# Performance work log

Measured on AMD Instinct MI355X. Metric: run time of the kernel, lower is better.

Reference implementation:

```python
import jax, jax.numpy as jnp
import numpy as np

EMBED_DIM = 256
NUM_HEADS = 8
HEAD_DIM = EMBED_DIM // NUM_HEADS


def setup_inputs() -> dict:
    key0 = jax.random.key(0)
    ks = jax.random.split(key0, 12)
    B, T, S, E = 4, 256, 16384, EMBED_DIM
    inv = 1.0 / np.sqrt(E)
    inputs = {
        "query": jax.random.normal(ks[0], (B, T, E), dtype=jnp.float32),
        "key": jax.random.normal(ks[1], (B, S, E), dtype=jnp.float32),
        "value": jax.random.normal(ks[2], (B, S, E), dtype=jnp.float32),
        "mask": jax.random.uniform(ks[3], (B, T, S), dtype=jnp.float32),
        # nn.MultiheadAttention in-projection (split into q/k/v parts) and out-projection
        "Wq": jax.random.uniform(ks[4], (E, E), jnp.float32, -inv, inv),
        "bq": jnp.zeros((E,), jnp.float32),
        "Wk": jax.random.uniform(ks[5], (E, E), jnp.float32, -inv, inv),
        "bk": jnp.zeros((E,), jnp.float32),
        "Wv": jax.random.uniform(ks[6], (E, E), jnp.float32, -inv, inv),
        "bv": jnp.zeros((E,), jnp.float32),
        "Wo": jax.random.uniform(ks[7], (E, E), jnp.float32, -inv, inv),
        "bo": jnp.zeros((E,), jnp.float32),
        # fixed default scaling factors (num_heads must be 8)
        "scaling_factors": jnp.asarray([32.0, 32.0, 16.0, 16.0, 8.0, 8.0, 4.0, 4.0], jnp.float32),
    }
    return inputs


def reference(query, key, value, mask, Wq, bq, Wk, bk, Wv, bv, Wo, bo, scaling_factors):
    B, T, E = query.shape
    S = key.shape[1]
    H, D = NUM_HEADS, HEAD_DIM
    # input projections (torch Linear convention: x @ W.T + b)
    q = (query @ Wq.T + bq).reshape(B, T, H, D).transpose(0, 2, 1, 3)  # [B,H,T,D]
    k = (key @ Wk.T + bk).reshape(B, S, H, D).transpose(0, 2, 1, 3)    # [B,H,S,D]
    v = (value @ Wv.T + bv).reshape(B, S, H, D).transpose(0, 2, 1, 3)  # [B,H,S,D]
    scale = 1.0 / jnp.sqrt(jnp.asarray(D, query.dtype))
    scores = jnp.einsum("bhtd,bhsd->bhts", q * scale, k)               # [B,H,T,S]
    # per-head scaled soft mask added as attention bias
    bias = mask[:, None, :, :] * scaling_factors[None, :, None, None]  # [B,H,T,S]
    attn = jax.nn.softmax(scores + bias, axis=-1)
    out = jnp.einsum("bhts,bhsd->bhtd", attn, v)                       # [B,H,T,D]
    out = out.transpose(0, 2, 1, 3).reshape(B, T, E)
    return out @ Wo.T + bo
```

## Files before the change

### kernel.cpp

```cpp
#include <hip/hip_runtime.h>

#define B_ 4
#define T_ 256
#define S_ 16384
#define E_ 256
#define H_ 8
#define D_ 32

typedef _Float16 f16;
typedef _Float16 f16x2 __attribute__((ext_vector_type(2)));
typedef _Float16 f16x4 __attribute__((ext_vector_type(4)));
typedef _Float16 f16x8 __attribute__((ext_vector_type(8)));
typedef float f32x4 __attribute__((ext_vector_type(4)));

typedef const __attribute__((address_space(1))) void* gas_t;
typedef __attribute__((address_space(3))) void* las_t;

__device__ __forceinline__ void gload_lds16(const void* g, void* l) {
    __builtin_amdgcn_global_load_lds((gas_t)g, (las_t)l, 16, 0, 0);
}

__device__ __forceinline__ f16x2 cvt_pk_f16(float a, float b) {
    return __builtin_bit_cast(f16x2, __builtin_amdgcn_cvt_pkrtz(a, b));
}

#define LOG2E 1.4426950408889634f

__global__ void cvt_w4_kernel(const float* __restrict__ wa, const float* __restrict__ wb,
                              const float* __restrict__ wc, const float* __restrict__ wd,
                              f16* __restrict__ oa, f16* __restrict__ ob,
                              f16* __restrict__ oc, f16* __restrict__ od) {
    int m = blockIdx.y;
    const float* src = m == 0 ? wa : m == 1 ? wb : m == 2 ? wc : wd;
    f16* dst = m == 0 ? oa : m == 1 ? ob : m == 2 ? oc : od;
    int i = (blockIdx.x * 256 + threadIdx.x) * 4;
    float4 v = *(const float4*)(src + i);
    f16x4 h = {(f16)v.x, (f16)v.y, (f16)v.z, (f16)v.w};
    *(f16x4*)(dst + i) = h;
}

template <bool OUT16>
__device__ __forceinline__ void qproj_body(
    f16* SMEM, const float* __restrict__ in, const f16* __restrict__ w16,
    const float* __restrict__ bias, void* __restrict__ outp, int bid, float oscale)
{
    f16 (*As)[264] = (f16(*)[264])SMEM;
    f16 (*Bs)[264] = (f16(*)[264])(SMEM + 32 * 264);
    int tid = threadIdx.x;
    int wq = tid >> 6, ln = tid & 63, g = ln >> 4, lc = ln & 15;
    int row0 = (bid & 31) * 32;
    int n0 = (bid >> 5) * 32;
    {
        int r = tid >> 3, q0 = (tid & 7) * 32;
        const float* ip = in + (size_t)(row0 + r) * 256 + q0;
        #pragma unroll
        for (int i = 0; i < 8; i++) {
            float4 v = *(const float4*)(ip + i * 4);
            f16x4 hv = {(f16)v.x, (f16)v.y, (f16)v.z, (f16)v.w};
            *(f16x4*)&As[r][q0 + i * 4] = hv;
        }
        const f16* wp = w16 + (size_t)(n0 + r) * 256 + q0;
        #pragma unroll
        for (int i = 0; i < 4; i++)
            *(f16x8*)&Bs[r][q0 + i * 8] = *(const f16x8*)(wp + i * 8);
    }
    __syncthreads();
    int mi = wq >> 1, ni = wq & 1;
    f32x4 acc = {0.f, 0.f, 0.f, 0.f};
    #pragma unroll
    for (int ks = 0; ks < 8; ks++) {
        f16x8 a = *(const f16x8*)&As[mi * 16 + lc][ks * 32 + g * 8];
        f16x8 bf = *(const f16x8*)&Bs[ni * 16 + lc][ks * 32 + g * 8];
        acc = __builtin_amdgcn_mfma_f32_16x16x32_f16(a, bf, acc, 0, 0, 0);
    }
    int n = n0 + ni * 16 + lc;
    float bv = bias[n];
    #pragma unroll
    for (int r = 0; r < 4; r++) {
        int row = row0 + mi * 16 + g * 4 + r;
        float val = (acc[r] + bv) * oscale;
        if (OUT16) ((f16*)outp)[(size_t)row * 256 + n] = (f16)val;
        else       ((float*)outp)[(size_t)row * 256 + n] = val;
    }
}

template <int MODE>
__device__ __forceinline__ void proj_body(
    f16* SMEM, const float* __restrict__ in, const f16* __restrict__ w16,
    const float* __restrict__ bias, void* __restrict__ outp, int bx, float oscale)
{
    f16 (*As)[64][40] = (f16(*)[64][40])&SMEM[0];
    f16* BsF = &SMEM[5120];
    int tid = threadIdx.x;
    int wv = tid >> 6, ln = tid & 63, g = ln >> 4, lc = ln & 15;
    int row0 = bx * 64;

    f32x4 acc[4][4];
    #pragma unroll
    for (int i = 0; i < 4; i++)
        #pragma unroll
        for (int j = 0; j < 4; j++) acc[i][j] = (f32x4){0.f, 0.f, 0.f, 0.f};

    auto stage = [&](int kb, int bufi) {
        int m = tid >> 3, kq = (tid & 7) << 2;
        #pragma unroll
        for (int h2 = 0; h2 < 2; h2++) {
            int mm = m + h2 * 32;
            float4 v = *(const float4*)(in + (size_t)(row0 + mm) * 256 + kb + kq);
            f16x4 hv = {(f16)v.x, (f16)v.y, (f16)v.z, (f16)v.w};
            *(f16x4*)&As[bufi][mm][kq] = hv;
        }
        #pragma unroll
        for (int c4 = 0; c4 < 4; c4++) {
            int cc = wv * 4 + c4;
            int row = cc * 16 + (ln >> 2);
            int sj = (ln & 3) ^ ((row >> 1) & 3);
            gload_lds16(w16 + (size_t)row * 256 + kb + sj * 8,
                        (char*)BsF + bufi * 16384 + cc * 1024);
        }
    };

    stage(0, 0);
    __syncthreads();
    #pragma unroll 1
    for (int ks = 0; ks < 8; ks++) {
        if (ks < 7) stage((ks + 1) * 32, (ks + 1) & 1);
        int bufi = ks & 1;
        f16x8 af[4], bf[4];
        #pragma unroll
        for (int mi = 0; mi < 4; mi++) af[mi] = *(const f16x8*)&As[bufi][mi * 16 + lc][g * 8];
        #pragma unroll
        for (int ni = 0; ni < 4; ni++) {
            int n = wv * 64 + ni * 16 + lc;
            bf[ni] = *(const f16x8*)&BsF[bufi * 8192 + n * 32 + ((g ^ ((n >> 1) & 3)) << 3)];
        }
        #pragma unroll
        for (int mi = 0; mi < 4; mi++)
            #pragma unroll
            for (int ni = 0; ni < 4; ni++)
                acc[mi][ni] = __builtin_amdgcn_mfma_f32_16x16x32_f16(af[mi], bf[ni], acc[mi][ni], 0, 0, 0);
        __syncthreads();
    }

    if (MODE == 1) {
        #pragma unroll
        for (int ni = 0; ni < 4; ni++) {
            int n = wv * 64 + ni * 16 + lc;
            float bv = bias[n];
            #pragma unroll
            for (int mi = 0; mi < 4; mi++) {
                #pragma unroll
                for (int r = 0; r < 4; r++) {
                    int row = row0 + mi * 16 + g * 4 + r;
                    ((f16*)outp)[(size_t)row * 256 + n] = (f16)((acc[mi][ni][r] + bv) * oscale);
                }
            }
        }
    } else {
        f16* TR = &SMEM[0];
        __syncthreads();
        #pragma unroll
        for (int ni = 0; ni < 4; ni++) {
            int n = wv * 64 + ni * 16 + lc;
            float bv = bias[n];
            #pragma unroll
            for (int mi = 0; mi < 4; mi++) {
                f16x4 hv;
                #pragma unroll
                for (int r = 0; r < 4; r++) hv[r] = (f16)((acc[mi][ni][r] + bv) * oscale);
                *(f16x4*)&TR[n * 68 + mi * 16 + g * 4] = hv;
            }
        }
        __syncthreads();
        int bb = row0 >> 14, sbase = row0 & 16383;
        f16* vout = (f16*)outp;
        #pragma unroll
        for (int p = 0; p < 4; p++) {
            int n = p * 64 + wv * 16 + (ln >> 2);
            int sc = (ln & 3) * 16;
            f16x8 v0 = *(const f16x8*)&TR[n * 68 + sc];
            f16x8 v1 = *(const f16x8*)&TR[n * 68 + sc + 8];
            f16* op = vout + ((size_t)(bb * 256 + n)) * 16384 + sbase + sc;
            *(f16x8*)op = v0;
            *(f16x8*)(op + 8) = v1;
        }
    }
}

__global__ __launch_bounds__(256, 3) void proj_fused(
    const float* __restrict__ query, const float* __restrict__ key, const float* __restrict__ value,
    const f16* __restrict__ Wq16, const f16* __restrict__ Wk16, const f16* __restrict__ Wv16,
    const float* __restrict__ bq, const float* __restrict__ bk, const float* __restrict__ bv,
    f16* __restrict__ q16, f16* __restrict__ k16, f16* __restrict__ v16T, float qscale)
{
    __shared__ __align__(16) f16 SMEM[21504];
    int bx = blockIdx.x;
    if (bx < 1024) {
        proj_body<1>(SMEM, key, Wk16, bk, k16, bx, 1.0f);
    } else if (bx < 2048) {
        proj_body<2>(SMEM, value, Wv16, bv, v16T, bx - 1024, 1.0f);
    } else {
        qproj_body<true>(SMEM, query, Wq16, bq, q16, bx - 2048, qscale);
    }
}

__global__ __launch_bounds__(256, 4) void out_proj(
    const float* __restrict__ in, const f16* __restrict__ w16,
    const float* __restrict__ bias, void* __restrict__ outp)
{
    __shared__ __align__(16) f16 SMEM[16896];
    qproj_body<false>(SMEM, in, w16, bias, outp, blockIdx.x + blockIdx.y * 32, 1.0f);
}

__global__ __launch_bounds__(1024, 4) void attn_kernel(
    const f16* __restrict__ q16,
    const f16* __restrict__ k16,
    const f16* __restrict__ v16T,
    const float* __restrict__ mask,
    const float* __restrict__ scal,
    float* __restrict__ partO, float* __restrict__ partL)
{
    constexpr int ITERS = 16;
    __shared__ __align__(16) f16 KT[3][32 * 256];
    __shared__ __align__(16) f16 VT[3][256 * 32];
    __shared__ __align__(16) float MT[3][128 * 32];

    int raw = blockIdx.x;
    int th = raw >> 7, b = (raw >> 5) & 3, ck = raw & 31;
    int tid = threadIdx.x;
    int wv = tid >> 6;
    int h = wv & 7, tsub = wv >> 3;
    int ln = tid & 63, g = ln >> 4, lc = ln & 15;
    int t0 = th * 128, s0 = ck * 512;

    float sc_h = scal[h] * LOG2E;
    float negfix = -(sc_h + 4.0f);

    f16x8 qf[4];
    #pragma unroll
    for (int tl = 0; tl < 4; tl++) {
        const f16* qp = q16 + (size_t)(b * T_ + t0 + tsub * 64 + tl * 16 + lc) * E_ + h * 32 + g * 8;
        qf[tl] = *(const f16x8*)qp;
    }

    f32x4 oac[4][2];
    float l_part[4];
    #pragma unroll
    for (int tl = 0; tl < 4; tl++) {
        oac[tl][0] = (f32x4){0.f, 0.f, 0.f, 0.f};
        oac[tl][1] = (f32x4){0.f, 0.f, 0.f, 0.f};
        l_part[tl] = 0.f;
    }

    auto stage = [&](int it, int bufi) {
        int sg0 = s0 + it * 32;
        {
            int sl = wv * 2 + (ln >> 5);
            int slot = (sl ^ (sl >> 3)) & 7;
            int jc = (ln & 31) ^ slot;
            gload_lds16(k16 + (size_t)(b * S_ + sg0 + sl) * E_ + jc * 8,
                        (char*)&KT[bufi][0] + wv * 1024);
        }
        {
            int dl = wv * 16 + (ln >> 2);
            int srcj = (ln & 3) ^ ((dl >> 1) & 3);
            gload_lds16(v16T + (size_t)(b * E_ + dl) * S_ + sg0 + srcj * 8,
                        (char*)&VT[bufi][0] + wv * 1024);
        }
        {
            int r = ln >> 3;
            int sj = (ln & 7) ^ r;
            gload_lds16(mask + (size_t)(b * T_ + t0 + wv * 8 + r) * S_ + sg0 + sj * 4,
                        (char*)&MT[bufi][0] + wv * 1024);
        }
    };

    stage(0, 0);
    stage(1, 1);

    f32x4 zero4 = {0.f, 0.f, 0.f, 0.f};
    int ib = 0;

    #pragma unroll 1
    for (int it = 0; it < ITERS; it++) {
        if (it + 1 < ITERS) { asm volatile("s_waitcnt vmcnt(3)" ::: "memory"); }
        else                { asm volatile("s_waitcnt vmcnt(0)" ::: "memory"); }
        __builtin_amdgcn_s_barrier();
        asm volatile("" ::: "memory");
        if (it + 2 < ITERS) {
            int wb = ib + 2; if (wb >= 3) wb -= 3;
            stage(it + 2, wb);
        }

        f16x8 kb[2];
        #pragma unroll
        for (int si = 0; si < 2; si++) {
            int sl = si * 16 + lc;
            int slot = (sl ^ (sl >> 3)) & 7;
            int j = (h * 4 + g) ^ slot;
            kb[si] = *(const f16x8*)((char*)&KT[ib][0] + sl * 512 + j * 16);
        }
        f16x4 va[2][2];
        #pragma unroll
        for (int si = 0; si < 2; si++) {
            #pragma unroll
            for (int ni = 0; ni < 2; ni++) {
                int d = h * 32 + ni * 16 + lc;
                int u = (si * 2 + (g >> 1)) ^ ((d >> 1) & 3);
                va[si][ni] = *(const f16x4*)((char*)&VT[ib][0] + d * 64 + u * 16 + (g & 1) * 8);
            }
        }

        #pragma unroll
        for (int tl = 0; tl < 4; tl++) {
            int t = tsub * 64 + tl * 16 + lc;
            const float4 mf0 = *(const float4*)((char*)&MT[ib][0] + t * 128 + (((g    ) ^ (t & 7)) << 4));
            const float4 mf1 = *(const float4*)((char*)&MT[ib][0] + t * 128 + (((4 + g) ^ (t & 7)) << 4));
            f32x4 st0 = __builtin_amdgcn_mfma_f32_16x16x32_f16(kb[0], qf[tl], zero4, 0, 0, 0);
            f32x4 st1 = __builtin_amdgcn_mfma_f32_16x16x32_f16(kb[1], qf[tl], zero4, 0, 0, 0);
            float p0 = __builtin_amdgcn_exp2f(st0[0] + __builtin_fmaf(mf0.x, sc_h, negfix));
            float p1 = __builtin_amdgcn_exp2f(st0[1] + __builtin_fmaf(mf0.y, sc_h, negfix));
            float p2 = __builtin_amdgcn_exp2f(st0[2] + __builtin_fmaf(mf0.z, sc_h, negfix));
            float p3 = __builtin_amdgcn_exp2f(st0[3] + __builtin_fmaf(mf0.w, sc_h, negfix));
            float p4 = __builtin_amdgcn_exp2f(st1[0] + __builtin_fmaf(mf1.x, sc_h, negfix));
            float p5 = __builtin_amdgcn_exp2f(st1[1] + __builtin_fmaf(mf1.y, sc_h, negfix));
            float p6 = __builtin_amdgcn_exp2f(st1[2] + __builtin_fmaf(mf1.z, sc_h, negfix));
            float p7 = __builtin_amdgcn_exp2f(st1[3] + __builtin_fmaf(mf1.w, sc_h, negfix));
            l_part[tl] += ((p0 + p1) + (p2 + p3)) + ((p4 + p5) + (p6 + p7));
            f16x2 c01 = cvt_pk_f16(p0, p1);
            f16x2 c23 = cvt_pk_f16(p2, p3);
            f16x2 c45 = cvt_pk_f16(p4, p5);
            f16x2 c67 = cvt_pk_f16(p6, p7);
            f16x4 pb0 = {c01[0], c01[1], c23[0], c23[1]};
            f16x4 pb1 = {c45[0], c45[1], c67[0], c67[1]};
            oac[tl][0] = __builtin_amdgcn_mfma_f32_16x16x16f16(va[0][0], pb0, oac[tl][0], 0, 0, 0);
            oac[tl][0] = __builtin_amdgcn_mfma_f32_16x16x16f16(va[1][0], pb1, oac[tl][0], 0, 0, 0);
            oac[tl][1] = __builtin_amdgcn_mfma_f32_16x16x16f16(va[0][1], pb0, oac[tl][1], 0, 0, 0);
            oac[tl][1] = __builtin_amdgcn_mfma_f32_16x16x16f16(va[1][1], pb1, oac[tl][1], 0, 0, 0);
        }
        ib++; if (ib >= 3) ib -= 3;
    }

    #pragma unroll
    for (int tl = 0; tl < 4; tl++) {
        float lv = l_part[tl];
        lv += __shfl_xor(lv, 16, 64);
        lv += __shfl_xor(lv, 32, 64);
        l_part[tl] = lv;
    }
    float* po = partO + (size_t)raw * 128 * 256;
    #pragma unroll
    for (int tl = 0; tl < 4; tl++) {
        #pragma unroll
        for (int ni = 0; ni < 2; ni++) {
            float4 o4 = {oac[tl][ni][0], oac[tl][ni][1], oac[tl][ni][2], oac[tl][ni][3]};
            *(float4*)(po + (size_t)(tsub * 64 + tl * 16 + lc) * 256 + h * 32 + ni * 16 + g * 4) = o4;
        }
    }
    if (g == 0) {
        float* pl = partL + (size_t)raw * 128 * 8;
        #pragma unroll
        for (int tl = 0; tl < 4; tl++) {
            int trow = tsub * 64 + tl * 16 + lc;
            pl[trow * 8 + h] = l_part[tl];
        }
    }
}

__global__ __launch_bounds__(256) void combine_kernel(
    const float* __restrict__ partO, const float* __restrict__ partL,
    float* __restrict__ attnO)
{
    int bid = blockIdx.x;
    int b = bid >> 8, t = bid & 255;
    int th = t >> 7, tl = t & 127;
    int tid = threadIdx.x;
    __shared__ float sl[32][8];
    {
        int ck = tid >> 3, hh = tid & 7;
        size_t blk = (size_t)(th * 128 + b * 32 + ck);
        sl[ck][hh] = partL[blk * 1024 + tl * 8 + hh];
    }
    __syncthreads();
    int h = tid >> 5;
    float L = 0.f;
    #pragma unroll 8
    for (int ck = 0; ck < 32; ck++) L += sl[ck][h];
    float acc = 0.f;
    #pragma unroll 4
    for (int ck = 0; ck < 32; ck++) {
        size_t blk = (size_t)(th * 128 + b * 32 + ck);
        acc += partO[blk * 32768 + (size_t)tl * 256 + tid];
    }
    attnO[(size_t)bid * 256 + tid] = acc / L;
}

extern "C" void kernel_launch(void* const* d_in, const int* in_sizes, int n_in,
                              void* d_out, int out_size, void* d_ws, size_t ws_size,
                              hipStream_t stream) {
    (void)in_sizes; (void)n_in; (void)out_size; (void)ws_size;
    const float* query = (const float*)d_in[0];
    const float* key   = (const float*)d_in[1];
    const float* value = (const float*)d_in[2];
    const float* mask  = (const float*)d_in[3];
    const float* Wq = (const float*)d_in[4];
    const float* bq = (const float*)d_in[5];
    const float* Wk = (const float*)d_in[6];
    const float* bk = (const float*)d_in[7];
    const float* Wv = (const float*)d_in[8];
    const float* bv = (const float*)d_in[9];
    const float* Wo = (const float*)d_in[10];
    const float* bo = (const float*)d_in[11];
    const float* scal = (const float*)d_in[12];

    char* ws = (char*)d_ws;
    f16* Wq16 = (f16*)(ws + 0);
    f16* Wk16 = (f16*)(ws + (1 << 17));
    f16* Wv16 = (f16*)(ws + (2 << 17));
    f16* Wo16 = (f16*)(ws + (3 << 17));
    f16* q16  = (f16*)(ws + (4 << 17));
    float* attnO = (float*)(ws + 1048576);
    f16* k16  = (f16*)(ws + 2097152);
    f16* v16T = (f16*)(ws + 35651584);
    float* partO = (float*)(ws + 69206016);
    float* partL = (float*)(ws + 103809024);

    cvt_w4_kernel<<<dim3(64, 4), 256, 0, stream>>>(Wq, Wk, Wv, Wo, Wq16, Wk16, Wv16, Wo16);

    const float qscale = 0.17677669529663687f * LOG2E;
    proj_fused<<<2304, 256, 0, stream>>>(query, key, value, Wq16, Wk16, Wv16,
                                         bq, bk, bv, q16, k16, v16T, qscale);

    attn_kernel<<<256, 1024, 0, stream>>>(q16, k16, v16T, mask, scal, partO, partL);
    combine_kernel<<<1024, 256, 0, stream>>>(partO, partL, attnO);

    out_proj<<<dim3(32, 8), 256, 0, stream>>>(attnO, Wo16, bo, (float*)d_out);
}
```

Baseline: 126.3 us.

## Rewrite K/V/Q projection with register-resident weights and pipelined activation staging

Replaces the projection kernel with a 512-thread design. Each wave loads its 32-column slice of the fp32 weight once, converts it to fp16 in registers, and keeps it there. 128-row activation tiles stream through a triple-buffered swizzled LDS ring, with explicit vmcnt waits so the next loads overlap the MFMAs. This removes the separate weight-conversion kernel, the per-k-step weight staging and the LDS transpose for V^T, whose stores are now written straight from MFMA fragments with operands swapped. The out projection also reads fp32 Wo directly and converts it inline. The cost is high register pressure from the cached weights and hand-tuned waitcnt sequencing that must match the real load ordering.

```diff
diff --git a/kernel.cpp b/kernel.cpp
--- a/kernel.cpp
+++ b/kernel.cpp
@@ -24,28 +24,140 @@
     return __builtin_bit_cast(f16x2, __builtin_amdgcn_cvt_pkrtz(a, b));
 }
 
+__device__ __forceinline__ f16x8 pack8(float4 a, float4 b) {
+    f16x2 p0 = cvt_pk_f16(a.x, a.y), p1 = cvt_pk_f16(a.z, a.w);
+    f16x2 p2 = cvt_pk_f16(b.x, b.y), p3 = cvt_pk_f16(b.z, b.w);
+    return (f16x8){p0[0], p0[1], p1[0], p1[1], p2[0], p2[1], p3[0], p3[1]};
+}
+
 #define LOG2E 1.4426950408889634f
 
-__global__ void cvt_w4_kernel(const float* __restrict__ wa, const float* __restrict__ wb,
-                              const float* __restrict__ wc, const float* __restrict__ wd,
-                              f16* __restrict__ oa, f16* __restrict__ ob,
-                              f16* __restrict__ oc, f16* __restrict__ od) {
-    int m = blockIdx.y;
-    const float* src = m == 0 ? wa : m == 1 ? wb : m == 2 ? wc : wd;
-    f16* dst = m == 0 ? oa : m == 1 ? ob : m == 2 ? oc : od;
-    int i = (blockIdx.x * 256 + threadIdx.x) * 4;
-    float4 v = *(const float4*)(src + i);
-    f16x4 h = {(f16)v.x, (f16)v.y, (f16)v.z, (f16)v.w};
-    *(f16x4*)(dst + i) = h;
-}
-
-template <bool OUT16>
-__device__ __forceinline__ void qproj_body(
-    f16* SMEM, const float* __restrict__ in, const f16* __restrict__ w16,
-    const float* __restrict__ bias, void* __restrict__ outp, int bid, float oscale)
+template <int MODE>
+__device__ __forceinline__ void proj2_body(
+    char* lbase, const float* __restrict__ in, const float* __restrict__ W,
+    const float* __restrict__ bias, f16* __restrict__ out, int row0, float oscale)
 {
+    constexpr int NT = 8;
+    int tid = threadIdx.x;
+    int wv = tid >> 6, ln = tid & 63, g = ln >> 4, lc = ln & 15;
+
+    f16x8 wf[2][8];
+    #pragma unroll
+    for (int ni = 0; ni < 2; ni++) {
+        const float* wp = W + (size_t)(wv * 32 + ni * 16 + lc) * 256 + g * 8;
+        #pragma unroll
+        for (int ks = 0; ks < 8; ks++) {
+            float4 a = *(const float4*)(wp + ks * 32);
+            float4 b = *(const float4*)(wp + ks * 32 + 4);
+            wf[ni][ks] = pack8(a, b);
+        }
+    }
+    float bl[2][4], bn[2];
+    if (MODE == 1) {
+        #pragma unroll
+        for (int ni = 0; ni < 2; ni++) bn[ni] = bias[wv * 32 + ni * 16 + lc];
+    } else {
+        #pragma unroll
+        for (int ni = 0; ni < 2; ni++)
+            #pragma unroll
+            for (int r = 0; r < 4; r++) bl[ni][r] = bias[wv * 32 + ni * 16 + g * 4 + r];
+    }
+
+    int srow = tid >> 5, sc = tid & 31;
+    int scs = (sc & 24) | ((sc ^ srow) & 7);
+    const float* gsrc = in + (size_t)(row0 + srow) * 256 + sc * 8;
+    int ldoff = srow * 512 + scs * 16;
+    int bb = row0 >> 14, sbase = row0 & 16383;
+
+    float4 r0[NT], r1[NT];
+    auto issue = [&](int t) {
+        const float* p = gsrc + (size_t)t * 4096;
+        r0[t] = *(const float4*)p;
+        r1[t] = *(const float4*)(p + 4);
+    };
+    auto wr = [&](int t) {
+        *(f16x8*)(lbase + (t % 3) * 8192 + ldoff) = pack8(r0[t], r1[t]);
+    };
+
+    issue(0); issue(1);
+    asm volatile("s_waitcnt vmcnt(2)" ::: "memory");
+    wr(0);
+    issue(2);
+    asm volatile("s_waitcnt vmcnt(2)" ::: "memory");
+    wr(1);
+    asm volatile("s_waitcnt lgkmcnt(0)" ::: "memory");
+    __builtin_amdgcn_s_barrier();
+
+    #pragma unroll
+    for (int t = 0; t < NT; t++) {
+        f32x4 a0 = {0.f, 0.f, 0.f, 0.f}, a1 = {0.f, 0.f, 0.f, 0.f};
+        #pragma unroll
+        for (int ks = 0; ks < 8; ks++) {
+            int c = ks * 4 + g;
+            int cs = (c & 24) | ((c ^ lc) & 7);
+            f16x8 af = *(const f16x8*)(lbase + (t % 3) * 8192 + lc * 512 + cs * 16);
+            if (MODE == 1) {
+                a0 = __builtin_amdgcn_mfma_f32_16x16x32_f16(af, wf[0][ks], a0, 0, 0, 0);
+                a1 = __builtin_amdgcn_mfma_f32_16x16x32_f16(af, wf[1][ks], a1, 0, 0, 0);
+            } else {
+                a0 = __builtin_amdgcn_mfma_f32_16x16x32_f16(wf[0][ks], af, a0, 0, 0, 0);
+                a1 = __builtin_amdgcn_mfma_f32_16x16x32_f16(wf[1][ks], af, a1, 0, 0, 0);
+            }
+        }
+        if (MODE == 1) {
+            f16x4 h0, h1;
+            #pragma unroll
+            for (int r = 0; r < 4; r++) {
+                h0[r] = (f16)(a0[r] + bn[0]);
+                h1[r] = (f16)(a1[r] + bn[1]);
+            }
+            int s = sbase + t * 16 + g * 4;
+            *(f16x4*)(out + ((size_t)(bb * 256 + wv * 32 + lc) << 14) + s) = h0;
+            *(f16x4*)(out + ((size_t)(bb * 256 + wv * 32 + 16 + lc) << 14) + s) = h1;
+        } else {
+            f16x4 h0, h1;
+            #pragma unroll
+            for (int r = 0; r < 4; r++) {
+                h0[r] = (f16)((a0[r] + bl[0][r]) * oscale);
+                h1[r] = (f16)((a1[r] + bl[1][r]) * oscale);
+            }
+            size_t rowb = (size_t)(row0 + t * 16 + lc) * 256;
+            *(f16x4*)(out + rowb + wv * 32 + g * 4) = h0;
+            *(f16x4*)(out + rowb + wv * 32 + 16 + g * 4) = h1;
+        }
+        if (t + 3 < NT) issue(t + 3);
+        if (t + 2 < NT) {
+            if (t + 3 < NT) { asm volatile("s_waitcnt vmcnt(4)" ::: "memory"); }
+            else            { asm volatile("s_waitcnt vmcnt(2)" ::: "memory"); }
+            wr(t + 2);
+            asm volatile("s_waitcnt lgkmcnt(0)" ::: "memory");
+            __builtin_amdgcn_s_barrier();
+        }
+    }
+}
+
+__global__ __launch_bounds__(512, 4) void proj_fused2(
+    const float* __restrict__ query, const float* __restrict__ key, const float* __restrict__ value,
+    const float* __restrict__ Wq, const float* __restrict__ Wk, const float* __restrict__ Wv,
+    const float* __restrict__ bq, const float* __restrict__ bk, const float* __restrict__ bv,
+    f16* __restrict__ q16, f16* __restrict__ k16, f16* __restrict__ v16T, float qscale)
+{
+    __shared__ __align__(16) f16 AT[3][4096];
+    char* lb = (char*)&AT[0][0];
+    int bx = blockIdx.x;
+    if (bx < 512)       proj2_body<0>(lb, key,   Wk, bk, k16,  bx * 128, 1.0f);
+    else if (bx < 1024) proj2_body<1>(lb, value, Wv, bv, v16T, (bx - 512) * 128, 1.0f);
+    else                proj2_body<2>(lb, query, Wq, bq, q16,  (bx - 1024) * 128, qscale);
+}
+
+__global__ __launch_bounds__(256, 4) void out_proj(
+    const float* __restrict__ in, const float* __restrict__ w,
+    const float* __restrict__ bias, float* __restrict__ outp)
+{
+    __shared__ __align__(16) f16 SMEM[16896];
     f16 (*As)[264] = (f16(*)[264])SMEM;
     f16 (*Bs)[264] = (f16(*)[264])(SMEM + 32 * 264);
+    int bid = blockIdx.x + blockIdx.y * 32;
     int tid = threadIdx.x;
     int wq = tid >> 6, ln = tid & 63, g = ln >> 4, lc = ln & 15;
     int row0 = (bid & 31) * 32;
@@ -54,15 +166,18 @@
         int r = tid >> 3, q0 = (tid & 7) * 32;
         const float* ip = in + (size_t)(row0 + r) * 256 + q0;
         #pragma unroll
-        for (int i = 0; i < 8; i++) {
-            float4 v = *(const float4*)(ip + i * 4);
-            f16x4 hv = {(f16)v.x, (f16)v.y, (f16)v.z, (f16)v.w};
-            *(f16x4*)&As[r][q0 + i * 4] = hv;
-        }
-        const f16* wp = w16 + (size_t)(n0 + r) * 256 + q0;
-        #pragma unroll
-        for (int i = 0; i < 4; i++)
-            *(f16x8*)&Bs[r][q0 + i * 8] = *(const f16x8*)(wp + i * 8);
+        for (int i = 0; i < 4; i++) {
+            float4 v0 = *(const float4*)(ip + i * 8);
+            float4 v1 = *(const float4*)(ip + i * 8 + 4);
+            *(f16x8*)&As[r][q0 + i * 8] = pack8(v0, v1);
+        }
+        const float* wp = w + (size_t)(n0 + r) * 256 + q0;
+        #pragma unroll
+        for (int i = 0; i < 4; i++) {
+            float4 v0 = *(const float4*)(wp + i * 8);
+            float4 v1 = *(const float4*)(wp + i * 8 + 4);
+            *(f16x8*)&Bs[r][q0 + i * 8] = pack8(v0, v1);
+        }
     }
     __syncthreads();
     int mi = wq >> 1, ni = wq & 1;
@@ -78,138 +193,8 @@
     #pragma unroll
     for (int r = 0; r < 4; r++) {
         int row = row0 + mi * 16 + g * 4 + r;
-        float val = (acc[r] + bv) * oscale;
-        if (OUT16) ((f16*)outp)[(size_t)row * 256 + n] = (f16)val;
-        else       ((float*)outp)[(size_t)row * 256 + n] = val;
-    }
-}
-
-template <int MODE>
-__device__ __forceinline__ void proj_body(
-    f16* SMEM, const float* __restrict__ in, const f16* __restrict__ w16,
-    const float* __restrict__ bias, void* __restrict__ outp, int bx, float oscale)
-{
-    f16 (*As)[64][40] = (f16(*)[64][40])&SMEM[0];
-    f16* BsF = &SMEM[5120];
-    int tid = threadIdx.x;
-    int wv = tid >> 6, ln = tid & 63, g = ln >> 4, lc = ln & 15;
-    int row0 = bx * 64;
-
-    f32x4 acc[4][4];
-    #pragma unroll
-    for (int i = 0; i < 4; i++)
-        #pragma unroll
-        for (int j = 0; j < 4; j++) acc[i][j] = (f32x4){0.f, 0.f, 0.f, 0.f};
-
-    auto stage = [&](int kb, int bufi) {
-        int m = tid >> 3, kq = (tid & 7) << 2;
-        #pragma unroll
-        for (int h2 = 0; h2 < 2; h2++) {
-            int mm = m + h2 * 32;
-            float4 v = *(const float4*)(in + (size_t)(row0 + mm) * 256 + kb + kq);
-            f16x4 hv = {(f16)v.x, (f16)v.y, (f16)v.z, (f16)v.w};
-            *(f16x4*)&As[bufi][mm][kq] = hv;
-        }
-        #pragma unroll
-        for (int c4 = 0; c4 < 4; c4++) {
-            int cc = wv * 4 + c4;
-            int row = cc * 16 + (ln >> 2);
-            int sj = (ln & 3) ^ ((row >> 1) & 3);
-            gload_lds16(w16 + (size_t)row * 256 + kb + sj * 8,
-                        (char*)BsF + bufi * 16384 + cc * 1024);
-        }
-    };
-
-    stage(0, 0);
-    __syncthreads();
-    #pragma unroll 1
-    for (int ks = 0; ks < 8; ks++) {
-        if (ks < 7) stage((ks + 1) * 32, (ks + 1) & 1);
-        int bufi = ks & 1;
-        f16x8 af[4], bf[4];
-        #pragma unroll
-        for (int mi = 0; mi < 4; mi++) af[mi] = *(const f16x8*)&As[bufi][mi * 16 + lc][g * 8];
-        #pragma unroll
-        for (int ni = 0; ni < 4; ni++) {
-            int n = wv * 64 + ni * 16 + lc;
-            bf[ni] = *(const f16x8*)&BsF[bufi * 8192 + n * 32 + ((g ^ ((n >> 1) & 3)) << 3)];
-        }
-        #pragma unroll
-        for (int mi = 0; mi < 4; mi++)
-            #pragma unroll
-            for (int ni = 0; ni < 4; ni++)
-                acc[mi][ni] = __builtin_amdgcn_mfma_f32_16x16x32_f16(af[mi], bf[ni], acc[mi][ni], 0, 0, 0);
-        __syncthreads();
-    }
-
-    if (MODE == 1) {
-        #pragma unroll
-        for (int ni = 0; ni < 4; ni++) {
-            int n = wv * 64 + ni * 16 + lc;
-            float bv = bias[n];
-            #pragma unroll
-            for (int mi = 0; mi < 4; mi++) {
-                #pragma unroll
-                for (int r = 0; r < 4; r++) {
-                    int row = row0 + mi * 16 + g * 4 + r;
-                    ((f16*)outp)[(size_t)row * 256 + n] = (f16)((acc[mi][ni][r] + bv) * oscale);
-                }
-            }
-        }
-    } else {
-        f16* TR = &SMEM[0];
-        __syncthreads();
-        #pragma unroll
-        for (int ni = 0; ni < 4; ni++) {
-            int n = wv * 64 + ni * 16 + lc;
-            float bv = bias[n];
-            #pragma unroll
-            for (int mi = 0; mi < 4; mi++) {
-                f16x4 hv;
-                #pragma unroll
-                for (int r = 0; r < 4; r++) hv[r] = (f16)((acc[mi][ni][r] + bv) * oscale);
-                *(f16x4*)&TR[n * 68 + mi * 16 + g * 4] = hv;
-            }
-        }
-        __syncthreads();
-        int bb = row0 >> 14, sbase = row0 & 16383;
-        f16* vout = (f16*)outp;
-        #pragma unroll
-        for (int p = 0; p < 4; p++) {
-            int n = p * 64 + wv * 16 + (ln >> 2);
-            int sc = (ln & 3) * 16;
-            f16x8 v0 = *(const f16x8*)&TR[n * 68 + sc];
-            f16x8 v1 = *(const f16x8*)&TR[n * 68 + sc + 8];
-            f16* op = vout + ((size_t)(bb * 256 + n)) * 16384 + sbase + sc;
-            *(f16x8*)op = v0;
-            *(f16x8*)(op + 8) = v1;
-        }
-    }
-}
-
-__global__ __launch_bounds__(256, 3) void proj_fused(
-    const float* __restrict__ query, const float* __restrict__ key, const float* __restrict__ value,
-    const f16* __restrict__ Wq16, const f16* __restrict__ Wk16, const f16* __restrict__ Wv16,
-    const float* __restrict__ bq, const float* __restrict__ bk, const float* __restrict__ bv,
-    f16* __restrict__ q16, f16* __restrict__ k16, f16* __restrict__ v16T, float qscale)
-{
-    __shared__ __align__(16) f16 SMEM[21504];
-    int bx = blockIdx.x;
-    if (bx < 1024) {
-        proj_body<1>(SMEM, key, Wk16, bk, k16, bx, 1.0f);
-    } else if (bx < 2048) {
-        proj_body<2>(SMEM, value, Wv16, bv, v16T, bx - 1024, 1.0f);
-    } else {
-        qproj_body<true>(SMEM, query, Wq16, bq, q16, bx - 2048, qscale);
-    }
-}
-
-__global__ __launch_bounds__(256, 4) void out_proj(
-    const float* __restrict__ in, const f16* __restrict__ w16,
-    const float* __restrict__ bias, void* __restrict__ outp)
-{
-    __shared__ __align__(16) f16 SMEM[16896];
-    qproj_body<false>(SMEM, in, w16, bias, outp, blockIdx.x + blockIdx.y * 32, 1.0f);
+        outp[(size_t)row * 256 + n] = acc[r] + bv;
+    }
 }
 
 __global__ __launch_bounds__(1024, 4) void attn_kernel(
@@ -414,10 +399,6 @@
     const float* scal = (const float*)d_in[12];
 
     char* ws = (char*)d_ws;
-    f16* Wq16 = (f16*)(ws + 0);
-    f16* Wk16 = (f16*)(ws + (1 << 17));
-    f16* Wv16 = (f16*)(ws + (2 << 17));
-    f16* Wo16 = (f16*)(ws + (3 << 17));
     f16* q16  = (f16*)(ws + (4 << 17));
     float* attnO = (float*)(ws + 1048576);
     f16* k16  = (f16*)(ws + 2097152);
@@ -425,14 +406,12 @@
     float* partO = (float*)(ws + 69206016);
     float* partL = (float*)(ws + 103809024);
 
-    cvt_w4_kernel<<<dim3(64, 4), 256, 0, stream>>>(Wq, Wk, Wv, Wo, Wq16, Wk16, Wv16, Wo16);
-
     const float qscale = 0.17677669529663687f * LOG2E;
-    proj_fused<<<2304, 256, 0, stream>>>(query, key, value, Wq16, Wk16, Wv16,
-                                         bq, bk, bv, q16, k16, v16T, qscale);
+    proj_fused2<<<1032, 512, 0, stream>>>(query, key, value, Wq, Wk, Wv,
+                                          bq, bk, bv, q16, k16, v16T, qscale);
 
     attn_kernel<<<256, 1024, 0, stream>>>(q16, k16, v16T, mask, scal, partO, partL);
     combine_kernel<<<1024, 256, 0, stream>>>(partO, partL, attnO);
 
-    out_proj<<<dim3(32, 8), 256, 0, stream>>>(attnO, Wo16, bo, (float*)d_out);
-}
+    out_proj<<<dim3(32, 8), 256, 0, stream>>>(attnO, Wo, bo, (float*)d_out);
+}
```

New measurement: 147.9 us. +17.1%, slower.

## Register-prefetch K/V projection loads and read fp32 Wq/Wo directly

Applied to the files above, without the earlier changes.

The K/V projection main loop now prefetches activation tiles two steps ahead into registers and loads weight tiles one step ahead into LDS. It uses explicit vmcnt waits and a single barrier per step instead of two __syncthreads. The Q and output projections now read fp32 weights directly and convert them in-kernel, so the weight-conversion kernel handles only Wk and Wv. The aim is to hide global-load latency in the dominant projection kernel and cut conversion work, at the cost of more registers and hand-tuned wait counts.

```diff
diff --git a/kernel.cpp b/kernel.cpp
--- a/kernel.cpp
+++ b/kernel.cpp
@@ -16,6 +16,8 @@
 typedef const __attribute__((address_space(1))) void* gas_t;
 typedef __attribute__((address_space(3))) void* las_t;
 
+#define FENCE() asm volatile("" ::: "memory")
+
 __device__ __forceinline__ void gload_lds16(const void* g, void* l) {
     __builtin_amdgcn_global_load_lds((gas_t)g, (las_t)l, 16, 0, 0);
 }
@@ -24,15 +26,19 @@
     return __builtin_bit_cast(f16x2, __builtin_amdgcn_cvt_pkrtz(a, b));
 }
 
+__device__ __forceinline__ f16x8 pack8(float4 a, float4 b) {
+    f16x2 p0 = cvt_pk_f16(a.x, a.y), p1 = cvt_pk_f16(a.z, a.w);
+    f16x2 p2 = cvt_pk_f16(b.x, b.y), p3 = cvt_pk_f16(b.z, b.w);
+    return (f16x8){p0[0], p0[1], p1[0], p1[1], p2[0], p2[1], p3[0], p3[1]};
+}
+
 #define LOG2E 1.4426950408889634f
 
-__global__ void cvt_w4_kernel(const float* __restrict__ wa, const float* __restrict__ wb,
-                              const float* __restrict__ wc, const float* __restrict__ wd,
-                              f16* __restrict__ oa, f16* __restrict__ ob,
-                              f16* __restrict__ oc, f16* __restrict__ od) {
+__global__ void cvt_w2_kernel(const float* __restrict__ wa, const float* __restrict__ wb,
+                              f16* __restrict__ oa, f16* __restrict__ ob) {
     int m = blockIdx.y;
-    const float* src = m == 0 ? wa : m == 1 ? wb : m == 2 ? wc : wd;
-    f16* dst = m == 0 ? oa : m == 1 ? ob : m == 2 ? oc : od;
+    const float* src = m == 0 ? wa : wb;
+    f16* dst = m == 0 ? oa : ob;
     int i = (blockIdx.x * 256 + threadIdx.x) * 4;
     float4 v = *(const float4*)(src + i);
     f16x4 h = {(f16)v.x, (f16)v.y, (f16)v.z, (f16)v.w};
@@ -40,8 +46,8 @@
 }
 
 template <bool OUT16>
-__device__ __forceinline__ void qproj_body(
-    f16* SMEM, const float* __restrict__ in, const f16* __restrict__ w16,
+__device__ __forceinline__ void qproj32_body(
+    f16* SMEM, const float* __restrict__ in, const float* __restrict__ w,
     const float* __restrict__ bias, void* __restrict__ outp, int bid, float oscale)
 {
     f16 (*As)[264] = (f16(*)[264])SMEM;
@@ -54,15 +60,18 @@
         int r = tid >> 3, q0 = (tid & 7) * 32;
         const float* ip = in + (size_t)(row0 + r) * 256 + q0;
         #pragma unroll
-        for (int i = 0; i < 8; i++) {
-            float4 v = *(const float4*)(ip + i * 4);
-            f16x4 hv = {(f16)v.x, (f16)v.y, (f16)v.z, (f16)v.w};
-            *(f16x4*)&As[r][q0 + i * 4] = hv;
-        }
-        const f16* wp = w16 + (size_t)(n0 + r) * 256 + q0;
-        #pragma unroll
-        for (int i = 0; i < 4; i++)
-            *(f16x8*)&Bs[r][q0 + i * 8] = *(const f16x8*)(wp + i * 8);
+        for (int i = 0; i < 4; i++) {
+            float4 v0 = *(const float4*)(ip + i * 8);
+            float4 v1 = *(const float4*)(ip + i * 8 + 4);
+            *(f16x8*)&As[r][q0 + i * 8] = pack8(v0, v1);
+        }
+        const float* wp = w + (size_t)(n0 + r) * 256 + q0;
+        #pragma unroll
+        for (int i = 0; i < 4; i++) {
+            float4 v0 = *(const float4*)(wp + i * 8);
+            float4 v1 = *(const float4*)(wp + i * 8 + 4);
+            *(f16x8*)&Bs[r][q0 + i * 8] = pack8(v0, v1);
+        }
     }
     __syncthreads();
     int mi = wq >> 1, ni = wq & 1;
@@ -85,12 +94,12 @@
 }
 
 template <int MODE>
-__device__ __forceinline__ void proj_body(
-    f16* SMEM, const float* __restrict__ in, const f16* __restrict__ w16,
-    const float* __restrict__ bias, void* __restrict__ outp, int bx, float oscale)
-{
-    f16 (*As)[64][40] = (f16(*)[64][40])&SMEM[0];
-    f16* BsF = &SMEM[5120];
+__device__ __forceinline__ void proj_body4(
+    char* SMEM, const float* __restrict__ in, const f16* __restrict__ w16,
+    const float* __restrict__ bias, f16* __restrict__ out, int bx, float oscale)
+{
+    f16 (*As)[64][40] = (f16(*)[64][40])SMEM;
+    f16* Bs = (f16*)(SMEM + 10240);
     int tid = threadIdx.x;
     int wv = tid >> 6, ln = tid & 63, g = ln >> 4, lc = ln & 15;
     int row0 = bx * 64;
@@ -101,45 +110,63 @@
         #pragma unroll
         for (int j = 0; j < 4; j++) acc[i][j] = (f32x4){0.f, 0.f, 0.f, 0.f};
 
-    auto stage = [&](int kb, int bufi) {
-        int m = tid >> 3, kq = (tid & 7) << 2;
-        #pragma unroll
-        for (int h2 = 0; h2 < 2; h2++) {
-            int mm = m + h2 * 32;
-            float4 v = *(const float4*)(in + (size_t)(row0 + mm) * 256 + kb + kq);
-            f16x4 hv = {(f16)v.x, (f16)v.y, (f16)v.z, (f16)v.w};
-            *(f16x4*)&As[bufi][mm][kq] = hv;
-        }
+    int am = tid >> 3, akq = (tid & 7) << 2;
+    const float* abase = in + (size_t)(row0 + am) * 256 + akq;
+
+    float4 Ar[2][2];
+    auto issueA = [&](int t) {
+        const float* p = abase + t * 32;
+        Ar[t & 1][0] = *(const float4*)p;
+        Ar[t & 1][1] = *(const float4*)(p + (size_t)32 * 256);
+    };
+    auto wrA = [&](int t) {
+        float4 v0 = Ar[t & 1][0], v1 = Ar[t & 1][1];
+        f16x4 h0 = {(f16)v0.x, (f16)v0.y, (f16)v0.z, (f16)v0.w};
+        f16x4 h1 = {(f16)v1.x, (f16)v1.y, (f16)v1.z, (f16)v1.w};
+        *(f16x4*)&As[t & 1][am][akq] = h0;
+        *(f16x4*)&As[t & 1][am + 32][akq] = h1;
+    };
+    auto issueB = [&](int t) {
+        int kb = t * 32;
         #pragma unroll
         for (int c4 = 0; c4 < 4; c4++) {
             int cc = wv * 4 + c4;
             int row = cc * 16 + (ln >> 2);
             int sj = (ln & 3) ^ ((row >> 1) & 3);
             gload_lds16(w16 + (size_t)row * 256 + kb + sj * 8,
-                        (char*)BsF + bufi * 16384 + cc * 1024);
+                        (char*)Bs + (t & 1) * 16384 + cc * 1024);
         }
     };
 
-    stage(0, 0);
-    __syncthreads();
-    #pragma unroll 1
-    for (int ks = 0; ks < 8; ks++) {
-        if (ks < 7) stage((ks + 1) * 32, (ks + 1) & 1);
-        int bufi = ks & 1;
+    issueB(0);
+    FENCE();
+    issueA(0); issueA(1);
+    FENCE();
+
+    #pragma unroll
+    for (int t = 0; t < 8; t++) {
+        if (t < 7) { asm volatile("s_waitcnt vmcnt(2)" ::: "memory"); }
+        else       { asm volatile("s_waitcnt vmcnt(0)" ::: "memory"); }
+        wrA(t);
+        asm volatile("s_waitcnt lgkmcnt(0)" ::: "memory");
+        __builtin_amdgcn_s_barrier();
+        FENCE();
+        if (t + 1 < 8) { issueB(t + 1); FENCE(); }
+        if (t + 2 < 8) { issueA(t + 2); FENCE(); }
+
         f16x8 af[4], bf[4];
         #pragma unroll
-        for (int mi = 0; mi < 4; mi++) af[mi] = *(const f16x8*)&As[bufi][mi * 16 + lc][g * 8];
+        for (int mi = 0; mi < 4; mi++) af[mi] = *(const f16x8*)&As[t & 1][mi * 16 + lc][g * 8];
         #pragma unroll
         for (int ni = 0; ni < 4; ni++) {
             int n = wv * 64 + ni * 16 + lc;
-            bf[ni] = *(const f16x8*)&BsF[bufi * 8192 + n * 32 + ((g ^ ((n >> 1) & 3)) << 3)];
+            bf[ni] = *(const f16x8*)&Bs[(t & 1) * 8192 + n * 32 + ((g ^ ((n >> 1) & 3)) << 3)];
         }
         #pragma unroll
         for (int mi = 0; mi < 4; mi++)
             #pragma unroll
             for (int ni = 0; ni < 4; ni++)
                 acc[mi][ni] = __builtin_amdgcn_mfma_f32_16x16x32_f16(af[mi], bf[ni], acc[mi][ni], 0, 0, 0);
-        __syncthreads();
     }
 
     if (MODE == 1) {
@@ -152,12 +179,12 @@
                 #pragma unroll
                 for (int r = 0; r < 4; r++) {
                     int row = row0 + mi * 16 + g * 4 + r;
-                    ((f16*)outp)[(size_t)row * 256 + n] = (f16)((acc[mi][ni][r] + bv) * oscale);
+                    out[(size_t)row * 256 + n] = (f16)((acc[mi][ni][r] + bv) * oscale);
                 }
             }
         }
     } else {
-        f16* TR = &SMEM[0];
+        f16* TR = (f16*)SMEM;
         __syncthreads();
         #pragma unroll
         for (int ni = 0; ni < 4; ni++) {
@@ -173,43 +200,42 @@
         }
         __syncthreads();
         int bb = row0 >> 14, sbase = row0 & 16383;
-        f16* vout = (f16*)outp;
         #pragma unroll
         for (int p = 0; p < 4; p++) {
             int n = p * 64 + wv * 16 + (ln >> 2);
             int sc = (ln & 3) * 16;
             f16x8 v0 = *(const f16x8*)&TR[n * 68 + sc];
             f16x8 v1 = *(const f16x8*)&TR[n * 68 + sc + 8];
-            f16* op = vout + ((size_t)(bb * 256 + n)) * 16384 + sbase + sc;
+            f16* op = out + ((size_t)(bb * 256 + n)) * 16384 + sbase + sc;
             *(f16x8*)op = v0;
             *(f16x8*)(op + 8) = v1;
         }
     }
 }
 
-__global__ __launch_bounds__(256, 3) void proj_fused(
+__global__ __launch_bounds__(256, 3) void proj_fused4(
     const float* __restrict__ query, const float* __restrict__ key, const float* __restrict__ value,
-    const f16* __restrict__ Wq16, const f16* __restrict__ Wk16, const f16* __restrict__ Wv16,
+    const float* __restrict__ Wq, const f16* __restrict__ Wk16, const f16* __restrict__ Wv16,
     const float* __restrict__ bq, const float* __restrict__ bk, const float* __restrict__ bv,
     f16* __restrict__ q16, f16* __restrict__ k16, f16* __restrict__ v16T, float qscale)
 {
-    __shared__ __align__(16) f16 SMEM[21504];
+    __shared__ __align__(16) char SMEM[43008];
     int bx = blockIdx.x;
     if (bx < 1024) {
-        proj_body<1>(SMEM, key, Wk16, bk, k16, bx, 1.0f);
+        proj_body4<1>(SMEM, key, Wk16, bk, k16, bx, 1.0f);
     } else if (bx < 2048) {
-        proj_body<2>(SMEM, value, Wv16, bv, v16T, bx - 1024, 1.0f);
+        proj_body4<2>(SMEM, value, Wv16, bv, v16T, bx - 1024, 1.0f);
     } else {
-        qproj_body<true>(SMEM, query, Wq16, bq, q16, bx - 2048, qscale);
+        qproj32_body<true>((f16*)SMEM, query, Wq, bq, q16, bx - 2048, qscale);
     }
 }
 
 __global__ __launch_bounds__(256, 4) void out_proj(
-    const float* __restrict__ in, const f16* __restrict__ w16,
-    const float* __restrict__ bias, void* __restrict__ outp)
+    const float* __restrict__ in, const float* __restrict__ w,
+    const float* __restrict__ bias, float* __restrict__ outp)
 {
     __shared__ __align__(16) f16 SMEM[16896];
-    qproj_body<false>(SMEM, in, w16, bias, outp, blockIdx.x + blockIdx.y * 32, 1.0f);
+    qproj32_body<false>(SMEM, in, w, bias, outp, blockIdx.x + blockIdx.y * 32, 1.0f);
 }
 
 __global__ __launch_bounds__(1024, 4) void attn_kernel(
@@ -286,7 +312,7 @@
         if (it + 1 < ITERS) { asm volatile("s_waitcnt vmcnt(3)" ::: "memory"); }
         else                { asm volatile("s_waitcnt vmcnt(0)" ::: "memory"); }
         __builtin_amdgcn_s_barrier();
-        asm volatile("" ::: "memory");
+        FENCE();
         if (it + 2 < ITERS) {
             int wb = ib + 2; if (wb >= 3) wb -= 3;
             stage(it + 2, wb);
@@ -414,10 +440,8 @@
     const float* scal = (const float*)d_in[12];
 
     char* ws = (char*)d_ws;
-    f16* Wq16 = (f16*)(ws + 0);
-    f16* Wk16 = (f16*)(ws + (1 << 17));
-    f16* Wv16 = (f16*)(ws + (2 << 17));
-    f16* Wo16 = (f16*)(ws + (3 << 17));
+    f16* Wk16 = (f16*)(ws + 0);
+    f16* Wv16 = (f16*)(ws + (1 << 17));
     f16* q16  = (f16*)(ws + (4 << 17));
     float* attnO = (float*)(ws + 1048576);
     f16* k16  = (f16*)(ws + 2097152);
@@ -425,14 +449,14 @@
     float* partO = (float*)(ws + 69206016);
     float* partL = (float*)(ws + 103809024);
 
-    cvt_w4_kernel<<<dim3(64, 4), 256, 0, stream>>>(Wq, Wk, Wv, Wo, Wq16, Wk16, Wv16, Wo16);
+    cvt_w2_kernel<<<dim3(64, 2), 256, 0, stream>>>(Wk, Wv, Wk16, Wv16);
 
     const float qscale = 0.17677669529663687f * LOG2E;
-    proj_fused<<<2304, 256, 0, stream>>>(query, key, value, Wq16, Wk16, Wv16,
-                                         bq, bk, bv, q16, k16, v16T, qscale);
+    proj_fused4<<<2304, 256, 0, stream>>>(query, key, value, Wq, Wk16, Wv16,
+                                          bq, bk, bv, q16, k16, v16T, qscale);
 
     attn_kernel<<<256, 1024, 0, stream>>>(q16, k16, v16T, mask, scal, partO, partL);
     combine_kernel<<<1024, 256, 0, stream>>>(partO, partL, attnO);
 
-    out_proj<<<dim3(32, 8), 256, 0, stream>>>(attnO, Wo16, bo, (float*)d_out);
-}
+    out_proj<<<dim3(32, 8), 256, 0, stream>>>(attnO, Wo, bo, (float*)d_out);
+}
```

After: 127.3 us. No clear change (+0.8%).
